# Optimization experiments

Measured on AMD Instinct MI355X. Metric: run time of the kernel, lower is better.

The kernel has to match this reference:

```python
import jax, jax.numpy as jnp
import numpy as np

B, SENSORY, STATE, MOTOR = 4096, 64, 128, 32
ODE_UNFOLDS = 6
EPS = 1e-8
ELAPSED_TIME = 1.0


def setup_inputs() -> dict:
    key = jax.random.key(0)
    ks = jax.random.split(key, 20)
    u = lambda k, shape, lo, hi: jax.random.uniform(k, shape, jnp.float32, lo, hi)
    sign = lambda k, shape: jnp.where(jax.random.bernoulli(k, 0.5, shape), 1.0, -1.0).astype(jnp.float32)
    mask = lambda k, shape: (jax.random.uniform(k, shape) < 0.75).astype(jnp.float32)
    return {
        "inputs": jax.random.normal(ks[0], (B, SENSORY), jnp.float32),
        "states": jax.random.normal(ks[1], (B, STATE), jnp.float32),
        "gleak": u(ks[2], (STATE,), 0.001, 1.0),
        "vleak": u(ks[3], (STATE,), -0.2, 0.2),
        "cm": u(ks[4], (STATE,), 0.4, 0.6),
        "w": u(ks[5], (STATE, STATE), 0.001, 1.0),
        "sigma": u(ks[6], (STATE, STATE), 3.0, 8.0),
        "mu": u(ks[7], (STATE, STATE), 0.3, 0.8),
        "erev": sign(ks[8], (STATE, STATE)),
        "sensory_w": u(ks[9], (SENSORY, STATE), 0.001, 1.0),
        "sensory_sigma": u(ks[10], (SENSORY, STATE), 3.0, 8.0),
        "sensory_mu": u(ks[11], (SENSORY, STATE), 0.3, 0.8),
        "sensory_erev": sign(ks[12], (SENSORY, STATE)),
        "sparsity_mask": mask(ks[13], (STATE, STATE)),
        "sensory_sparsity_mask": mask(ks[14], (SENSORY, STATE)),
        "input_w": jnp.ones((SENSORY,), jnp.float32),
        "input_b": jnp.zeros((SENSORY,), jnp.float32),
        "output_w": jnp.ones((MOTOR,), jnp.float32),
        "output_b": jnp.zeros((MOTOR,), jnp.float32),
    }


def _syn_sigmoid(v_pre, mu, sigma):
    # v_pre: [B, P] -> [B, P, 1]; mu/sigma: [P, S]
    return jax.nn.sigmoid(sigma * (v_pre[..., None] - mu))


def reference(inputs, states, gleak, vleak, cm, w, sigma, mu, erev,
              sensory_w, sensory_sigma, sensory_mu, sensory_erev,
              sparsity_mask, sensory_sparsity_mask,
              input_w, input_b, output_w, output_b):
    # input mapping (affine); make_positive_fn = Identity (explicit constraints)
    x = inputs * input_w + input_b

    # sensory contributions (computed once, shared across unfolds)
    sens_act = sensory_w * _syn_sigmoid(x, sensory_mu, sensory_sigma)  # [B, In, S]
    sens_act = sens_act * sensory_sparsity_mask
    w_num_sensory = jnp.sum(sens_act * sensory_erev, axis=1)  # [B, S]
    w_den_sensory = jnp.sum(sens_act, axis=1)                 # [B, S]

    cm_t = cm / (ELAPSED_TIME / ODE_UNFOLDS)  # [S]

    v_pre = states
    for _ in range(ODE_UNFOLDS):
        w_act = w * _syn_sigmoid(v_pre, mu, sigma)   # [B, S, S]
        w_act = w_act * sparsity_mask
        w_numerator = jnp.sum(w_act * erev, axis=1) + w_num_sensory
        w_denominator = jnp.sum(w_act, axis=1) + w_den_sensory
        numerator = cm_t * v_pre + gleak * vleak + w_numerator
        denominator = cm_t + gleak + w_denominator
        v_pre = numerator / (denominator + EPS)

    # output mapping: slice motor neurons, then affine
    output = v_pre[:, :MOTOR] * output_w + output_b
    return output, v_pre
```

## Files before the change

### kernel.cpp

```cpp
#include <hip/hip_runtime.h>

#define LOG2E 1.4426950408889634f

constexpr int Bsz = 4096, Ssz = 128, Isz = 64, MOTOR = 32;
constexpr int BT = 4, NT = 256;

__global__ void ltc_prep(const float* __restrict__ w, const float* __restrict__ sigma,
                         const float* __restrict__ mu, const float* __restrict__ erev,
                         const float* __restrict__ smask,
                         const float* __restrict__ sw, const float* __restrict__ ssig,
                         const float* __restrict__ smu, const float* __restrict__ serev,
                         const float* __restrict__ ssmask,
                         float4* __restrict__ Tm, float4* __restrict__ Ts)
{
  int idx = blockIdx.x * blockDim.x + threadIdx.x;
  if (idx < 32 * Ssz) {
    int q = idx >> 7, s = idx & 127;
    float4 a, b, wv;
    #pragma unroll
    for (int jj = 0; jj < 4; ++jj) {
      int e = (q * 4 + jj) * Ssz + s;
      float sg = sigma[e];
      (&a.x)[jj] = -sg * LOG2E;
      (&b.x)[jj] = sg * mu[e] * LOG2E;
      (&wv.x)[jj] = w[e] * smask[e] * erev[e];
    }
    Tm[(q * 3 + 0) * Ssz + s] = a;
    Tm[(q * 3 + 1) * Ssz + s] = b;
    Tm[(q * 3 + 2) * Ssz + s] = wv;
  } else if (idx < 32 * Ssz + 16 * Ssz) {
    int k = idx - 32 * Ssz;
    int q = k >> 7, s = k & 127;
    float4 a, b, wv;
    #pragma unroll
    for (int jj = 0; jj < 4; ++jj) {
      int e = (q * 4 + jj) * Ssz + s;
      float sg = ssig[e];
      (&a.x)[jj] = -sg * LOG2E;
      (&b.x)[jj] = sg * smu[e] * LOG2E;
      (&wv.x)[jj] = sw[e] * ssmask[e] * serev[e];
    }
    Ts[(q * 3 + 0) * Ssz + s] = a;
    Ts[(q * 3 + 1) * Ssz + s] = b;
    Ts[(q * 3 + 2) * Ssz + s] = wv;
  }
}

__launch_bounds__(NT, 8)
__global__ void ltc_main(const float* __restrict__ inputs, const float* __restrict__ states,
                         const float* __restrict__ gleak, const float* __restrict__ vleak,
                         const float* __restrict__ cmv,
                         const float* __restrict__ iw, const float* __restrict__ ib,
                         const float* __restrict__ ow, const float* __restrict__ ob,
                         const float4* __restrict__ Tm, const float4* __restrict__ Ts,
                         float* __restrict__ out)
{
  __shared__ float vsh[BT][Ssz];
  __shared__ float xsh[BT][Isz];
  __shared__ float redn[2][2][Ssz];
  __shared__ float redd[2][2][Ssz];

  const int t = threadIdx.x;
  const int s = t & 127;
  const int h = t >> 7;
  const int b0 = blockIdx.x * BT;

  { int r = t >> 6, i = t & 63;
    xsh[r][i] = inputs[(b0 + r) * Isz + i] * iw[i] + ib[i]; }
  for (int k = t; k < BT * Ssz; k += NT) {
    int r = k >> 7, ss = k & 127;
    vsh[r][ss] = states[(b0 + r) * Ssz + ss];
  }
  const float cmt = cmv[s] * 6.0f;
  const float gl = gleak[s];
  const float gv = gl * vleak[s];
  const float dbase = cmt + gl + 1e-8f;
  __syncthreads();

  float sn[BT] = {0.f, 0.f, 0.f, 0.f}, sd[BT] = {0.f, 0.f, 0.f, 0.f};
  {
    const float4* pb = Ts + (h * 8 * 3 + 1) * Ssz + s;
    #pragma unroll 2
    for (int q = 0; q < 8; ++q) {
      float4 a4 = pb[-Ssz], b4 = pb[0], w4 = pb[Ssz];
      pb += 3 * Ssz;
      int col = (h * 8 + q) * 4;
      #pragma unroll
      for (int r = 0; r < BT; ++r) {
        float4 xq = *(const float4*)&xsh[r][col];
        #pragma unroll
        for (int jj = 0; jj < 4; ++jj) {
          float arg = fmaf((&a4.x)[jj], (&xq.x)[jj], (&b4.x)[jj]);
          float u = __builtin_amdgcn_exp2f(arg);
          float sig = __builtin_amdgcn_rcpf(1.0f + u);
          sn[r] = fmaf((&w4.x)[jj], sig, sn[r]);
          sd[r] = fmaf(fabsf((&w4.x)[jj]), sig, sd[r]);
        }
      }
    }
  }

  #pragma unroll 1
  for (int it = 0; it < 6; ++it) {
    float num[BT], den[BT];
    #pragma unroll
    for (int r = 0; r < BT; ++r) { num[r] = sn[r]; den[r] = sd[r]; }

    const float4* pb = Tm + (h * 16 * 3 + 1) * Ssz + s;
    #pragma unroll 2
    for (int q = 0; q < 16; ++q) {
      float4 a4 = pb[-Ssz], b4 = pb[0], w4 = pb[Ssz];
      pb += 3 * Ssz;
      int col = (h * 16 + q) * 4;
      #pragma unroll
      for (int r = 0; r < BT; ++r) {
        float4 vq = *(const float4*)&vsh[r][col];
        #pragma unroll
        for (int jj = 0; jj < 4; ++jj) {
          float arg = fmaf((&a4.x)[jj], (&vq.x)[jj], (&b4.x)[jj]);
          float u = __builtin_amdgcn_exp2f(arg);
          float sig = __builtin_amdgcn_rcpf(1.0f + u);
          num[r] = fmaf((&w4.x)[jj], sig, num[r]);
          den[r] = fmaf(fabsf((&w4.x)[jj]), sig, den[r]);
        }
      }
    }

    redn[h][0][s] = num[2 - 2 * h]; redn[h][1][s] = num[3 - 2 * h];
    redd[h][0][s] = den[2 - 2 * h]; redd[h][1][s] = den[3 - 2 * h];
    __syncthreads();
    #pragma unroll
    for (int k2 = 0; k2 < 2; ++k2) {
      int r = 2 * h + k2;
      float fn = num[r] + redn[1 - h][k2][s];
      float fd = den[r] + redd[1 - h][k2][s];
      float vo = vsh[r][s];
      vsh[r][s] = (fmaf(cmt, vo, gv) + fn) * __builtin_amdgcn_rcpf(dbase + fd);
    }
    __syncthreads();
  }

  for (int k = t; k < BT * Ssz; k += NT) {
    int r = k >> 7, ss = k & 127;
    out[Bsz * MOTOR + (b0 + r) * Ssz + ss] = vsh[r][ss];
  }
  if (t < BT * MOTOR) {
    int r = t >> 5, m = t & 31;
    out[(b0 + r) * MOTOR + m] = fmaf(vsh[r][m], ow[m], ob[m]);
  }
}

extern "C" void kernel_launch(void* const* d_in, const int* in_sizes, int n_in,
                              void* d_out, int out_size, void* d_ws, size_t ws_size,
                              hipStream_t stream) {
  const float* inputs = (const float*)d_in[0];
  const float* states = (const float*)d_in[1];
  const float* gleak  = (const float*)d_in[2];
  const float* vleak  = (const float*)d_in[3];
  const float* cmv    = (const float*)d_in[4];
  const float* w      = (const float*)d_in[5];
  const float* sigma  = (const float*)d_in[6];
  const float* mu     = (const float*)d_in[7];
  const float* erev   = (const float*)d_in[8];
  const float* sw     = (const float*)d_in[9];
  const float* ssig   = (const float*)d_in[10];
  const float* smu    = (const float*)d_in[11];
  const float* serev  = (const float*)d_in[12];
  const float* smask  = (const float*)d_in[13];
  const float* ssmask = (const float*)d_in[14];
  const float* iw     = (const float*)d_in[15];
  const float* ib     = (const float*)d_in[16];
  const float* ow     = (const float*)d_in[17];
  const float* ob     = (const float*)d_in[18];

  char* ws = (char*)d_ws;
  float4* Tm = (float4*)ws;
  float4* Ts = (float4*)(ws + 196608);
  float* out = (float*)d_out;

  constexpr int prep_items = 32 * Ssz + 16 * Ssz;
  ltc_prep<<<(prep_items + 255) / 256, 256, 0, stream>>>(
      w, sigma, mu, erev, smask, sw, ssig, smu, serev, ssmask, Tm, Ts);
  ltc_main<<<Bsz / BT, NT, 0, stream>>>(
      inputs, states, gleak, vleak, cmv, iw, ib, ow, ob, Tm, Ts, out);
}
```

Measured before the change: 119.5 us.

## Split batch rows across thread halves and double-buffer state to drop reduction

```diff
diff --git a/kernel.cpp b/kernel.cpp
--- a/kernel.cpp
+++ b/kernel.cpp
@@ -3,7 +3,7 @@
 #define LOG2E 1.4426950408889634f
 
 constexpr int Bsz = 4096, Ssz = 128, Isz = 64, MOTOR = 32;
-constexpr int BT = 4, NT = 256;
+constexpr int BT = 4, NT = 256, R = 2;
 
 __global__ void ltc_prep(const float* __restrict__ w, const float* __restrict__ sigma,
                          const float* __restrict__ mu, const float* __restrict__ erev,
@@ -46,7 +46,7 @@
   }
 }
 
-__launch_bounds__(NT, 8)
+__launch_bounds__(NT, 4)
 __global__ void ltc_main(const float* __restrict__ inputs, const float* __restrict__ states,
                          const float* __restrict__ gleak, const float* __restrict__ vleak,
                          const float* __restrict__ cmv,
@@ -55,21 +55,19 @@
                          const float4* __restrict__ Tm, const float4* __restrict__ Ts,
                          float* __restrict__ out)
 {
-  __shared__ float vsh[BT][Ssz];
+  __shared__ float vsh[2][BT][Ssz];
   __shared__ float xsh[BT][Isz];
-  __shared__ float redn[2][2][Ssz];
-  __shared__ float redd[2][2][Ssz];
 
   const int t = threadIdx.x;
   const int s = t & 127;
-  const int h = t >> 7;
+  const int r0 = (t >> 7) * R;
   const int b0 = blockIdx.x * BT;
 
   { int r = t >> 6, i = t & 63;
     xsh[r][i] = inputs[(b0 + r) * Isz + i] * iw[i] + ib[i]; }
   for (int k = t; k < BT * Ssz; k += NT) {
     int r = k >> 7, ss = k & 127;
-    vsh[r][ss] = states[(b0 + r) * Ssz + ss];
+    vsh[0][r][ss] = states[(b0 + r) * Ssz + ss];
   }
   const float cmt = cmv[s] * 6.0f;
   const float gl = gleak[s];
@@ -77,17 +75,16 @@
   const float dbase = cmt + gl + 1e-8f;
   __syncthreads();
 
-  float sn[BT] = {0.f, 0.f, 0.f, 0.f}, sd[BT] = {0.f, 0.f, 0.f, 0.f};
+  float sn[R] = {0.f, 0.f}, sd[R] = {0.f, 0.f};
   {
-    const float4* pb = Ts + (h * 8 * 3 + 1) * Ssz + s;
+    const float4* pb = Ts + 1 * Ssz + s;
     #pragma unroll 2
-    for (int q = 0; q < 8; ++q) {
+    for (int q = 0; q < 16; ++q) {
       float4 a4 = pb[-Ssz], b4 = pb[0], w4 = pb[Ssz];
       pb += 3 * Ssz;
-      int col = (h * 8 + q) * 4;
       #pragma unroll
-      for (int r = 0; r < BT; ++r) {
-        float4 xq = *(const float4*)&xsh[r][col];
+      for (int r = 0; r < R; ++r) {
+        float4 xq = *(const float4*)&xsh[r0 + r][q * 4];
         #pragma unroll
         for (int jj = 0; jj < 4; ++jj) {
           float arg = fmaf((&a4.x)[jj], (&xq.x)[jj], (&b4.x)[jj]);
@@ -102,19 +99,20 @@
 
   #pragma unroll 1
   for (int it = 0; it < 6; ++it) {
-    float num[BT], den[BT];
+    const int cur = it & 1;
+    const float* vcur = &vsh[cur][0][0];
+    float num[R], den[R];
     #pragma unroll
-    for (int r = 0; r < BT; ++r) { num[r] = sn[r]; den[r] = sd[r]; }
+    for (int r = 0; r < R; ++r) { num[r] = sn[r]; den[r] = sd[r]; }
 
-    const float4* pb = Tm + (h * 16 * 3 + 1) * Ssz + s;
+    const float4* pb = Tm + 1 * Ssz + s;
     #pragma unroll 2
-    for (int q = 0; q < 16; ++q) {
+    for (int q = 0; q < 32; ++q) {
       float4 a4 = pb[-Ssz], b4 = pb[0], w4 = pb[Ssz];
       pb += 3 * Ssz;
-      int col = (h * 16 + q) * 4;
       #pragma unroll
-      for (int r = 0; r < BT; ++r) {
-        float4 vq = *(const float4*)&vsh[r][col];
+      for (int r = 0; r < R; ++r) {
+        float4 vq = *(const float4*)&vcur[(r0 + r) * Ssz + q * 4];
         #pragma unroll
         for (int jj = 0; jj < 4; ++jj) {
           float arg = fmaf((&a4.x)[jj], (&vq.x)[jj], (&b4.x)[jj]);
@@ -126,27 +124,22 @@
       }
     }
 
-    redn[h][0][s] = num[2 - 2 * h]; redn[h][1][s] = num[3 - 2 * h];
-    redd[h][0][s] = den[2 - 2 * h]; redd[h][1][s] = den[3 - 2 * h];
-    __syncthreads();
     #pragma unroll
-    for (int k2 = 0; k2 < 2; ++k2) {
-      int r = 2 * h + k2;
-      float fn = num[r] + redn[1 - h][k2][s];
-      float fd = den[r] + redd[1 - h][k2][s];
-      float vo = vsh[r][s];
-      vsh[r][s] = (fmaf(cmt, vo, gv) + fn) * __builtin_amdgcn_rcpf(dbase + fd);
+    for (int r = 0; r < R; ++r) {
+      float vo = vcur[(r0 + r) * Ssz + s];
+      vsh[cur ^ 1][r0 + r][s] =
+          (fmaf(cmt, vo, gv) + num[r]) * __builtin_amdgcn_rcpf(dbase + den[r]);
     }
     __syncthreads();
   }
 
   for (int k = t; k < BT * Ssz; k += NT) {
     int r = k >> 7, ss = k & 127;
-    out[Bsz * MOTOR + (b0 + r) * Ssz + ss] = vsh[r][ss];
+    out[Bsz * MOTOR + (b0 + r) * Ssz + ss] = vsh[0][r][ss];
   }
   if (t < BT * MOTOR) {
     int r = t >> 5, m = t & 31;
-    out[(b0 + r) * MOTOR + m] = fmaf(vsh[r][m], ow[m], ob[m]);
+    out[(b0 + r) * MOTOR + m] = fmaf(vsh[0][r][m], ow[m], ob[m]);
   }
 }
 
```

Measured after the change: 113.6 us (median of 2 runs). 1.05x faster.
